# Performance work log

Hardware: AMD Instinct MI355X
Metric: run time of the kernel (lower is better)

## Reference

```python
import jax, jax.numpy as jnp
import numpy as np

B, S, D, H = 2, 2048, 1024, 16
HEAD_DIM = D // H
SCALE = HEAD_DIM ** -0.5


def setup_inputs() -> dict:
    key = jax.random.key(0)
    k1, k2, k3 = jax.random.split(key, 3)
    x = jax.random.normal(k1, (B, S, D), dtype=jnp.float32)
    # torch nn.Linear convention: weight is [out_features, in_features], y = x @ W.T + b
    W_qkv = jax.random.normal(k2, (3 * D, D), dtype=jnp.float32) * 0.02  # qkv Linear, bias=False
    W_out = jax.random.normal(k3, (D, D), dtype=jnp.float32) * 0.02
    b_out = jnp.zeros((D,), dtype=jnp.float32)
    return {"x": x, "W_qkv": W_qkv, "W_out": W_out, "b_out": b_out}


def reference(x, W_qkv, W_out, b_out):
    b, s, d_model = x.shape
    # qkv projection (no bias), then split 'b c (qkv h d) -> qkv b h c d'
    qkv = (x @ W_qkv.T).reshape(b, s, 3, H, HEAD_DIM).transpose(2, 0, 3, 1, 4)
    q, k, v = qkv[0], qkv[1], qkv[2]  # each [b, h, s, hd]
    # naive full attention: scores materialized as [b, h, s, s]
    attn = jax.nn.softmax(jnp.einsum('bhxd,bhyd->bhxy', q, k) * SCALE, axis=-1)
    # dropout is identity (rate 0 / eval mode)
    o = jnp.einsum('bhxy,bhyd->bhxd', attn, v)
    o = o.transpose(0, 2, 1, 3).reshape(b, s, d_model)  # 'b h c d -> b c (h d)'
    return o @ W_out.T + b_out
```

## Files before the change

kernel.cpp:

```cpp
#include <hip/hip_runtime.h>


typedef __attribute__((ext_vector_type(8))) short short8;
typedef __attribute__((ext_vector_type(4))) float f32x4;
typedef __attribute__((ext_vector_type(2))) unsigned int uint32x2;
typedef unsigned short ushort_t;
typedef unsigned int uint32;

#define AS1 __attribute__((address_space(1)))
#define AS3 __attribute__((address_space(3)))

__device__ __forceinline__ void gload_lds16(const void* gp, void* lp) {
    __builtin_amdgcn_global_load_lds((const AS1 void*)gp, (AS3 void*)lp, 16, 0, 0);
}

#if __has_builtin(__builtin_amdgcn_exp2f)
#define EXP2F(x) __builtin_amdgcn_exp2f(x)
#else
#define EXP2F(x) exp2f(x)
#endif

__device__ __forceinline__ uint32 rhu(float f) { return __float_as_uint(f) + 0x8000u; }
#if __has_builtin(__builtin_amdgcn_perm)
__device__ __forceinline__ uint32 pk2bf(float a, float b) {
    return __builtin_amdgcn_perm(rhu(b), rhu(a), 0x07060302u);
}
#else
__device__ __forceinline__ uint32 pk2bf(float a, float b) {
    return (rhu(a) >> 16) | (rhu(b) & 0xffff0000u);
}
#endif
__device__ __forceinline__ ushort_t f2bf(float f) { return (ushort_t)(rhu(f) >> 16); }

#if __has_builtin(__builtin_amdgcn_permlane32_swap)
__device__ __forceinline__ void plane32(uint32& a, uint32& b) {
    uint32x2 r = __builtin_amdgcn_permlane32_swap(a, b, false, false);
    a = r[0]; b = r[1];
}
#else
__device__ __forceinline__ void plane32(uint32& a, uint32& b) {
    asm("v_permlane32_swap_b32 %0, %1" : "+v"(a), "+v"(b));
}
#endif
#if __has_builtin(__builtin_amdgcn_permlane16_swap)
__device__ __forceinline__ void plane16(uint32& a, uint32& b) {
    uint32x2 r = __builtin_amdgcn_permlane16_swap(a, b, false, false);
    a = r[0]; b = r[1];
}
#else
__device__ __forceinline__ void plane16(uint32& a, uint32& b) {
    asm("v_permlane16_swap_b32 %0, %1" : "+v"(a), "+v"(b));
}
#endif

__global__ __launch_bounds__(256, 2)
void gemm_qkv(const float* __restrict__ A, const float* __restrict__ B,
              ushort_t* __restrict__ Cb, ushort_t* __restrict__ vT, float qScale) {
    __shared__ ushort_t lA[2][128 * 32];
    __shared__ ushort_t lB[2][192 * 32];
    const int K = 1024;
    const int tid = threadIdx.x;
    const int wave = tid >> 6, lane = tid & 63;
    const int quad = lane >> 4, l16 = lane & 15;
    const int rsw = (l16 >> 1) & 3;

    int bid = blockIdx.x + 16 * blockIdx.y;
    bid = (bid & 7) * 64 + (bid >> 3);
    const int nBase = (bid & 15) * 192, mBase = (bid >> 4) * 128;

    f32x4 acc[8][3];
#pragma unroll
    for (int i = 0; i < 8; i++)
#pragma unroll
        for (int j = 0; j < 3; j++) acc[i][j] = (f32x4){0.f, 0.f, 0.f, 0.f};

    const int srow = tid >> 2, slc = tid & 3;
    const int rs = (srow >> 1) & 3;
    const int gc = slc ^ rs;

    float4 ra[2][2], rb[3][2];

#define QLOAD(k0)                                                                     \
    {                                                                                 \
        _Pragma("unroll") for (int p = 0; p < 2; p++) {                               \
            const float* s = A + (size_t)(mBase + p * 64 + srow) * K + (k0) + gc * 8; \
            ra[p][0] = *(const float4*)(s);                                           \
            ra[p][1] = *(const float4*)(s + 4);                                       \
        }                                                                             \
        _Pragma("unroll") for (int p = 0; p < 3; p++) {                               \
            const float* s = B + (size_t)(nBase + p * 64 + srow) * K + (k0) + gc * 8; \
            rb[p][0] = *(const float4*)(s);                                           \
            rb[p][1] = *(const float4*)(s + 4);                                       \
        }                                                                             \
    }

#define QCVTW(buf)                                                                    \
    {                                                                                 \
        _Pragma("unroll") for (int p = 0; p < 2; p++) {                               \
            uint4 w;                                                                  \
            w.x = pk2bf(ra[p][0].x, ra[p][0].y); w.y = pk2bf(ra[p][0].z, ra[p][0].w); \
            w.z = pk2bf(ra[p][1].x, ra[p][1].y); w.w = pk2bf(ra[p][1].z, ra[p][1].w); \
            *(uint4*)(&lA[buf][(p * 64 + srow) * 32 + slc * 8]) = w;                  \
        }                                                                             \
        _Pragma("unroll") for (int p = 0; p < 3; p++) {                               \
            uint4 w;                                                                  \
            w.x = pk2bf(rb[p][0].x, rb[p][0].y); w.y = pk2bf(rb[p][0].z, rb[p][0].w); \
            w.z = pk2bf(rb[p][1].x, rb[p][1].y); w.w = pk2bf(rb[p][1].z, rb[p][1].w); \
            *(uint4*)(&lB[buf][(p * 64 + srow) * 32 + slc * 8]) = w;                  \
        }                                                                             \
    }

#define QCOMP(buf)                                                                    \
    {                                                                                 \
        short8 af[8], bf[3];                                                          \
        _Pragma("unroll") for (int i = 0; i < 8; i++)                                 \
            af[i] = *(const short8*)(&lA[buf][(i * 16 + l16) * 32 + ((quad ^ rsw) * 8)]); \
        _Pragma("unroll") for (int j = 0; j < 3; j++)                                 \
            bf[j] = *(const short8*)(&lB[buf][(wave * 48 + j * 16 + l16) * 32 +       \
                                              ((quad ^ rsw) * 8)]);                   \
        _Pragma("unroll") for (int i = 0; i < 8; i++)                                 \
            _Pragma("unroll") for (int j = 0; j < 3; j++)                             \
                acc[i][j] = __builtin_amdgcn_mfma_f32_16x16x32_bf16(af[i], bf[j],     \
                                                                    acc[i][j], 0, 0, 0); \
    }

    QLOAD(0);
    QCVTW(0);
    QLOAD(32);
    __syncthreads();

    for (int t = 0; t < 32; ++t) {
        const int buf = t & 1;
        QCOMP(buf);
        if (t < 31) {
            QCVTW(buf ^ 1);
            if (t < 30) QLOAD((t + 2) * 32);
        }
        __syncthreads();
    }

#pragma unroll
    for (int i = 0; i < 8; i++)
#pragma unroll
        for (int j = 0; j < 3; j++) {
            const int colBase = nBase + wave * 48 + j * 16;
            const int row0 = mBase + i * 16 + quad * 4;
            if (colBase >= 2048) {
                const int col = colBase + l16 - 2048;
                const int b = row0 >> 11, s0 = row0 & 2047;
                uint2 pk;
                pk.x = pk2bf(acc[i][j][0], acc[i][j][1]);
                pk.y = pk2bf(acc[i][j][2], acc[i][j][3]);
                *(uint2*)(vT + ((size_t)(b * 16) * 64 + col) * 2048 + s0) = pk;
            } else {
                const float cs = (colBase < 1024) ? qScale : 1.0f;
                const int col = colBase + l16;
#pragma unroll
                for (int r = 0; r < 4; r++)
                    Cb[(size_t)(row0 + r) * 2048 + col] = f2bf(acc[i][j][r] * cs);
            }
        }
}

__global__ __launch_bounds__(256, 2)
void gemm_out(const ushort_t* __restrict__ A, const float* __restrict__ B,
              float* __restrict__ Cf, const float* __restrict__ bias) {
    const int K = 1024, N = 1024;
    __shared__ ushort_t lA[2][64 * 64];
    __shared__ ushort_t lB[2][128 * 64];
    const int tid = threadIdx.x;
    const int wave = tid >> 6, lane = tid & 63;
    const int quad = lane >> 4, l16 = lane & 15;
    const int swz = l16 & 7;
    const int mBase = blockIdx.y * 64, nBase = blockIdx.x * 128;

    f32x4 acc[4][2];
#pragma unroll
    for (int i = 0; i < 4; i++)
#pragma unroll
        for (int j = 0; j < 2; j++) acc[i][j] = (f32x4){0.f, 0.f, 0.f, 0.f};

    const int srow = tid >> 3, slc = tid & 7;
    const int gc = slc ^ (srow & 7);

    short8 ra2[2];
    float4 rb[4][2];

#define OLOAD(k0)                                                                     \
    {                                                                                 \
        _Pragma("unroll") for (int c = 0; c < 2; c++)                                 \
            ra2[c] = *(const short8*)(A + (size_t)(mBase + c * 32 + srow) * K +       \
                                      (k0) + gc * 8);                                 \
        _Pragma("unroll") for (int p = 0; p < 4; p++) {                               \
            const float* s = B + (size_t)(nBase + p * 32 + srow) * K + (k0) + gc * 8; \
            rb[p][0] = *(const float4*)(s);                                           \
            rb[p][1] = *(const float4*)(s + 4);                                       \
        }                                                                             \
    }

#define OCVTW(buf)                                                                    \
    {                                                                                 \
        _Pragma("unroll") for (int c = 0; c < 2; c++)                                 \
            *(short8*)(&lA[buf][(c * 32 + srow) * 64 + slc * 8]) = ra2[c];            \
        _Pragma("unroll") for (int p = 0; p < 4; p++) {                               \
            uint4 w;                                                                  \
            w.x = pk2bf(rb[p][0].x, rb[p][0].y); w.y = pk2bf(rb[p][0].z, rb[p][0].w); \
            w.z = pk2bf(rb[p][1].x, rb[p][1].y); w.w = pk2bf(rb[p][1].z, rb[p][1].w); \
            *(uint4*)(&lB[buf][(p * 32 + srow) * 64 + slc * 8]) = w;                  \
        }                                                                             \
    }

#define OCOMP(buf)                                                                    \
    _Pragma("unroll") for (int ks = 0; ks < 2; ks++) {                                \
        short8 af[4], bf[2];                                                          \
        _Pragma("unroll") for (int i = 0; i < 4; i++)                                 \
            af[i] = *(const short8*)(&lA[buf][(i * 16 + l16) * 64 +                   \
                                              (((ks * 4 + quad) ^ swz) * 8)]);        \
        _Pragma("unroll") for (int j = 0; j < 2; j++)                                 \
            bf[j] = *(const short8*)(&lB[buf][(wave * 32 + j * 16 + l16) * 64 +       \
                                              (((ks * 4 + quad) ^ swz) * 8)]);        \
        _Pragma("unroll") for (int i = 0; i < 4; i++)                                 \
            _Pragma("unroll") for (int j = 0; j < 2; j++)                             \
                acc[i][j] = __builtin_amdgcn_mfma_f32_16x16x32_bf16(af[i], bf[j],     \
                                                                    acc[i][j], 0, 0, 0); \
    }

    OLOAD(0);
    OCVTW(0);
    OLOAD(64);
    __syncthreads();

    for (int t = 0; t < 16; ++t) {
        const int buf = t & 1;
        OCOMP(buf);
        if (t < 15) {
            OCVTW(buf ^ 1);
            if (t < 14) OLOAD((t + 2) * 64);
        }
        __syncthreads();
    }

#pragma unroll
    for (int i = 0; i < 4; i++)
#pragma unroll
        for (int j = 0; j < 2; j++)
#pragma unroll
            for (int r = 0; r < 4; r++) {
                const int row = mBase + i * 16 + quad * 4 + r;
                const int col = nBase + wave * 32 + j * 16 + l16;
                Cf[(size_t)row * N + col] = acc[i][j][r] + bias[col];
            }
}

__global__ __launch_bounds__(512, 4)
void attn_flash(const ushort_t* __restrict__ qk, const ushort_t* __restrict__ vT,
                ushort_t* __restrict__ o) {
    __shared__ ushort_t smem[28672];

    const int tid = threadIdx.x;
    const int wave = tid >> 6, lane = tid & 63;
    const int quad = lane >> 4, l16 = lane & 15;
    const int qg = wave & 3, kg = wave >> 2;
    const int bh = blockIdx.x, b = bh >> 4, h = bh & 15;
    const size_t rowBase = (size_t)b * 2048;
    const int qCol = h * 64, kCol = 1024 + h * 64;
    const int qRow0 = blockIdx.y * 128;
    const int swz = l16 & 7;

    const int sr = tid >> 3;
    const int sc = ((tid & 7) ^ (sr & 7)) * 8;

#pragma unroll
    for (int cc = 0; cc < 2; cc++)
        gload_lds16(qk + (rowBase + qRow0 + cc * 64 + sr) * 2048 + qCol + sc,
                    smem + 20480 + cc * 4096 + wave * 512);
    __syncthreads();
    short8 qf[2][2];
#pragma unroll
    for (int qt = 0; qt < 2; qt++)
#pragma unroll
        for (int ks = 0; ks < 2; ks++)
            qf[qt][ks] = *(const short8*)(smem + 20480 + (qg * 32 + qt * 16 + l16) * 64 +
                                          (((ks * 4 + quad) ^ swz) * 8));

    short8 onesA;
#pragma unroll
    for (int i = 0; i < 8; i++) onesA[i] = (short)0x3F80;

    f32x4 oacc[4][2];
    f32x4 lacc[2];
#pragma unroll
    for (int qt = 0; qt < 2; qt++) {
        lacc[qt] = (f32x4){0.f, 0.f, 0.f, 0.f};
#pragma unroll
        for (int dt = 0; dt < 4; dt++) oacc[dt][qt] = (f32x4){0.f, 0.f, 0.f, 0.f};
    }

    const ushort_t* kptr = qk + (rowBase + sr) * 2048 + kCol + sc;
    const ushort_t* vptr = vT + ((size_t)bh * 64 + sr) * 2048 + sc;

    f32x4 sacc[2][2];
    short8 pfA[2], pfB[2];

#define AT_STAGE(kbi, vbi, kt)                                                         \
    {                                                                                  \
        gload_lds16(kptr + (size_t)((kt) * 64) * 2048, smem + (kbi) * 4096 + wave * 512); \
        gload_lds16(vptr + (kt) * 64, smem + 8192 + (vbi) * 4096 + wave * 512);        \
    }

#define S_BLOCK(cur)                                                                   \
    {                                                                                  \
        const ushort_t* lK = smem + (cur) * 4096;                                      \
        _Pragma("unroll") for (int mh = 0; mh < 2; mh++) {                             \
            const int krow = kg * 32 + mh * 16 + l16;                                  \
            const short8 k0 = *(const short8*)(lK + krow * 64 + ((quad ^ swz) * 8));   \
            const short8 k1 = *(const short8*)(lK + krow * 64 + (((4 + quad) ^ swz) * 8)); \
            __builtin_amdgcn_s_setprio(1);                                             \
            _Pragma("unroll") for (int qt = 0; qt < 2; qt++) {                         \
                f32x4 t = (f32x4){0.f, 0.f, 0.f, 0.f};                                 \
                t = __builtin_amdgcn_mfma_f32_16x16x32_bf16(k0, qf[qt][0], t, 0, 0, 0); \
                t = __builtin_amdgcn_mfma_f32_16x16x32_bf16(k1, qf[qt][1], t, 0, 0, 0); \
                sacc[mh][qt] = t;                                                      \
            }                                                                          \
            __builtin_amdgcn_s_setprio(0);                                             \
        }                                                                              \
    }

#define EXPPK_BLOCK(pfdst)                                                             \
    _Pragma("unroll") for (int qt = 0; qt < 2; qt++) {                                 \
        uint32 a0 = pk2bf(EXP2F(sacc[0][qt][0]), EXP2F(sacc[0][qt][1]));               \
        uint32 a1 = pk2bf(EXP2F(sacc[0][qt][2]), EXP2F(sacc[0][qt][3]));               \
        uint32 b0 = pk2bf(EXP2F(sacc[1][qt][0]), EXP2F(sacc[1][qt][1]));               \
        uint32 b1 = pk2bf(EXP2F(sacc[1][qt][2]), EXP2F(sacc[1][qt][3]));               \
        plane32(a0, b0); plane16(a0, b0);                                              \
        plane32(a1, b1); plane16(a1, b1);                                              \
        union { uint32 u[4]; short8 s; } w_;                                           \
        w_.u[0] = a0; w_.u[1] = a1; w_.u[2] = b0; w_.u[3] = b1;                        \
        pfdst[qt] = w_.s;                                                              \
    }

#define PV_BLOCK(vbi, pf)                                                              \
    {                                                                                  \
        const ushort_t* lV = smem + 8192 + (vbi) * 4096;                               \
        _Pragma("unroll") for (int qt = 0; qt < 2; qt++)                               \
            lacc[qt] = __builtin_amdgcn_mfma_f32_16x16x32_bf16(onesA, pf[qt], lacc[qt], 0, 0, 0); \
        __builtin_amdgcn_s_setprio(1);                                                 \
        _Pragma("unroll") for (int dt = 0; dt < 4; dt++) {                             \
            const short8 vf = *(const short8*)(lV + (dt * 16 + l16) * 64 +             \
                                               (((kg * 4 + quad) ^ swz) * 8));         \
            _Pragma("unroll") for (int qt = 0; qt < 2; qt++)                           \
                oacc[dt][qt] = __builtin_amdgcn_mfma_f32_16x16x32_bf16(vf, pf[qt], oacc[dt][qt], 0, 0, 0); \
        }                                                                              \
        __builtin_amdgcn_s_setprio(0);                                                 \
    }

    AT_STAGE(0, 0, 0);

    __syncthreads();
    AT_STAGE(1, 1, 1);
    S_BLOCK(0);
    EXPPK_BLOCK(pfA);

    int vs = 2, vp = 0;
    for (int kt = 1; kt <= 29; kt += 2) {
        __syncthreads();
        AT_STAGE(0, vs, kt + 1);
        S_BLOCK(1);
        PV_BLOCK(vp, pfA);
        EXPPK_BLOCK(pfB);
        vs = (vs == 2) ? 0 : vs + 1;
        vp = (vp == 2) ? 0 : vp + 1;
        __syncthreads();
        AT_STAGE(1, vs, kt + 2);
        S_BLOCK(0);
        PV_BLOCK(vp, pfB);
        EXPPK_BLOCK(pfA);
        vs = (vs == 2) ? 0 : vs + 1;
        vp = (vp == 2) ? 0 : vp + 1;
    }

    __syncthreads();
    S_BLOCK(1);
    PV_BLOCK(0, pfA);
    EXPPK_BLOCK(pfB);
    PV_BLOCK(1, pfB);

    __syncthreads();
    float* red = (float*)smem;
    if (kg == 1) {
#pragma unroll
        for (int qt = 0; qt < 2; qt++) {
            if (quad == 0) red[8192 + qg * 32 + qt * 16 + l16] = lacc[qt][0];
#pragma unroll
            for (int dt = 0; dt < 4; dt++)
                *(f32x4*)(red + (((qg * 4 + dt) * 2 + qt) * 64 + lane) * 4) = oacc[dt][qt];
        }
    }
    __syncthreads();
    if (kg == 0) {
        float linv[2];
#pragma unroll
        for (int qt = 0; qt < 2; qt++)
            linv[qt] = 1.0f / (lacc[qt][0] + red[8192 + qg * 32 + qt * 16 + l16]);
#pragma unroll
        for (int qt = 0; qt < 2; qt++) {
            const size_t row = rowBase + qRow0 + qg * 32 + qt * 16 + l16;
#pragma unroll
            for (int dt = 0; dt < 4; dt++) {
                const f32x4 r = *(const f32x4*)(red + (((qg * 4 + dt) * 2 + qt) * 64 + lane) * 4);
                uint2 pk;
                pk.x = pk2bf((oacc[dt][qt][0] + r[0]) * linv[qt],
                             (oacc[dt][qt][1] + r[1]) * linv[qt]);
                pk.y = pk2bf((oacc[dt][qt][2] + r[2]) * linv[qt],
                             (oacc[dt][qt][3] + r[3]) * linv[qt]);
                *(uint2*)(o + row * 1024 + h * 64 + dt * 16 + quad * 4) = pk;
            }
        }
    }
}

extern "C" void kernel_launch(void* const* d_in, const int* in_sizes, int n_in,
                              void* d_out, int out_size, void* d_ws, size_t ws_size,
                              hipStream_t stream) {
    const float* x    = (const float*)d_in[0];
    const float* Wqkv = (const float*)d_in[1];
    const float* Wout = (const float*)d_in[2];
    const float* bout = (const float*)d_in[3];
    float* out = (float*)d_out;

    ushort_t* qkb = (ushort_t*)d_ws;
    ushort_t* vTb = qkb + (size_t)4096 * 2048;
    ushort_t* ob  = vTb + (size_t)32 * 64 * 2048;

    const float SC = 0.125f * 1.44269504089f;

    gemm_qkv<<<dim3(16, 32), 256, 0, stream>>>(x, Wqkv, qkb, vTb, SC);
    attn_flash<<<dim3(32, 16), 512, 0, stream>>>(qkb, vTb, ob);
    gemm_out<<<dim3(8, 64), 256, 0, stream>>>(ob, Wout, out, bout);
}
```

Baseline: 170.8 us.

## Deepen register prefetch to two stages in QKV and output GEMMs

Both projection GEMMs now keep two register staging sets (A/B) so global loads for tile t+2 and t+3 are in flight while tile t is computed, and the main loop is unrolled by two with fixed LDS buffer indices. This is meant to hide more global memory latency behind the MFMA work. It roughly doubles the staging register use, which could lower occupancy or cause spills, especially in the QKV kernel with its 8x3 accumulator tile.

```diff
diff --git a/kernel.cpp b/kernel.cpp
--- a/kernel.cpp
+++ b/kernel.cpp
@@ -78,9 +78,9 @@
     const int rs = (srow >> 1) & 3;
     const int gc = slc ^ rs;
 
-    float4 ra[2][2], rb[3][2];
-
-#define QLOAD(k0)                                                                     \
+    float4 raA[2][2], rbA[3][2], raB[2][2], rbB[3][2];
+
+#define QLOAD(ra, rb, k0)                                                             \
     {                                                                                 \
         _Pragma("unroll") for (int p = 0; p < 2; p++) {                               \
             const float* s = A + (size_t)(mBase + p * 64 + srow) * K + (k0) + gc * 8; \
@@ -94,7 +94,7 @@
         }                                                                             \
     }
 
-#define QCVTW(buf)                                                                    \
+#define QCVTW(ra, rb, buf)                                                            \
     {                                                                                 \
         _Pragma("unroll") for (int p = 0; p < 2; p++) {                               \
             uint4 w;                                                                  \
@@ -124,20 +124,26 @@
                                                                     acc[i][j], 0, 0, 0); \
     }
 
-    QLOAD(0);
-    QCVTW(0);
-    QLOAD(32);
-    __syncthreads();
-
-    for (int t = 0; t < 32; ++t) {
-        const int buf = t & 1;
-        QCOMP(buf);
-        if (t < 31) {
-            QCVTW(buf ^ 1);
-            if (t < 30) QLOAD((t + 2) * 32);
-        }
-        __syncthreads();
-    }
+    QLOAD(raA, rbA, 0);
+    QCVTW(raA, rbA, 0);
+    QLOAD(raB, rbB, 32);
+    QLOAD(raA, rbA, 64);
+    __syncthreads();
+
+    for (int t = 0; t < 30; t += 2) {
+        QCOMP(0);
+        QCVTW(raB, rbB, 1);
+        QLOAD(raB, rbB, (t + 3) * 32);
+        __syncthreads();
+        QCOMP(1);
+        QCVTW(raA, rbA, 0);
+        if (t < 28) QLOAD(raA, rbA, (t + 4) * 32);
+        __syncthreads();
+    }
+    QCOMP(0);
+    QCVTW(raB, rbB, 1);
+    __syncthreads();
+    QCOMP(1);
 
 #pragma unroll
     for (int i = 0; i < 8; i++)
@@ -181,24 +187,24 @@
         for (int j = 0; j < 2; j++) acc[i][j] = (f32x4){0.f, 0.f, 0.f, 0.f};
 
     const int srow = tid >> 3, slc = tid & 7;
-    const int gc = slc ^ (srow & 7);
-
-    short8 ra2[2];
-    float4 rb[4][2];
-
-#define OLOAD(k0)                                                                     \
+    const int gcc = slc ^ (srow & 7);
+
+    short8 raA2[2], raB2[2];
+    float4 rbA[4][2], rbB[4][2];
+
+#define OLOAD(ra2, rb, k0)                                                            \
     {                                                                                 \
         _Pragma("unroll") for (int c = 0; c < 2; c++)                                 \
             ra2[c] = *(const short8*)(A + (size_t)(mBase + c * 32 + srow) * K +       \
-                                      (k0) + gc * 8);                                 \
+                                      (k0) + gcc * 8);                                \
         _Pragma("unroll") for (int p = 0; p < 4; p++) {                               \
-            const float* s = B + (size_t)(nBase + p * 32 + srow) * K + (k0) + gc * 8; \
+            const float* s = B + (size_t)(nBase + p * 32 + srow) * K + (k0) + gcc * 8;\
             rb[p][0] = *(const float4*)(s);                                           \
             rb[p][1] = *(const float4*)(s + 4);                                       \
         }                                                                             \
     }
 
-#define OCVTW(buf)                                                                    \
+#define OCVTW(ra2, rb, buf)                                                           \
     {                                                                                 \
         _Pragma("unroll") for (int c = 0; c < 2; c++)                                 \
             *(short8*)(&lA[buf][(c * 32 + srow) * 64 + slc * 8]) = ra2[c];            \
@@ -225,20 +231,26 @@
                                                                     acc[i][j], 0, 0, 0); \
     }
 
-    OLOAD(0);
-    OCVTW(0);
-    OLOAD(64);
-    __syncthreads();
-
-    for (int t = 0; t < 16; ++t) {
-        const int buf = t & 1;
-        OCOMP(buf);
-        if (t < 15) {
-            OCVTW(buf ^ 1);
-            if (t < 14) OLOAD((t + 2) * 64);
-        }
-        __syncthreads();
-    }
+    OLOAD(raA2, rbA, 0);
+    OCVTW(raA2, rbA, 0);
+    OLOAD(raB2, rbB, 64);
+    OLOAD(raA2, rbA, 128);
+    __syncthreads();
+
+    for (int t = 0; t < 14; t += 2) {
+        OCOMP(0);
+        OCVTW(raB2, rbB, 1);
+        OLOAD(raB2, rbB, (t + 3) * 64);
+        __syncthreads();
+        OCOMP(1);
+        OCVTW(raA2, rbA, 0);
+        if (t < 12) OLOAD(raA2, rbA, (t + 4) * 64);
+        __syncthreads();
+    }
+    OCOMP(0);
+    OCVTW(raB2, rbB, 1);
+    __syncthreads();
+    OCOMP(1);
 
 #pragma unroll
     for (int i = 0; i < 4; i++)
```

After: 171.4 us. Within noise of the previous version (+0.3%).
